# Kernel optimization log

Hardware: AMD Instinct MI355X
Metric: run time of the kernel (lower is better)

## Reference

```python
import jax, jax.numpy as jnp
import numpy as np

CODEBOOK_SIZE = 8192
HIDDEN_SIZE = 256
N_ANCHORS = 5


def setup_inputs() -> dict:
    key = jax.random.key(0)
    k1, k2 = jax.random.split(key)
    z = jax.random.normal(k1, (8, 4096, HIDDEN_SIZE), dtype=jnp.float32)
    emb = 0.02 * jax.random.normal(k2, (CODEBOOK_SIZE, HIDDEN_SIZE), dtype=jnp.float32)
    # enforce_anchor_values(): first 5 rows are one-hot anchors (eye padded with zeros)
    anchors = jnp.zeros((N_ANCHORS, HIDDEN_SIZE), dtype=jnp.float32)
    anchors = anchors.at[:, :N_ANCHORS].set(jnp.eye(N_ANCHORS, dtype=jnp.float32))
    emb = emb.at[:N_ANCHORS, :].set(anchors)
    return {"z": z, "emb": emb}


def reference(z, emb):
    b, t, h = z.shape
    flat = z.reshape(b * t, h)
    # squared L2 distance: ||z||^2 - 2 z.e + ||e||^2  -> [b*t, K]
    dist = (
        jnp.sum(flat * flat, axis=1, keepdims=True)
        - 2.0 * (flat @ emb.T)
        + jnp.sum(emb * emb, axis=1)[None, :]
    )
    idx = jnp.argmin(dist, axis=1)  # [b*t]
    z_q = emb[idx].reshape(b, t, h)
    # straight-through estimator
    z_st = z + jax.lax.stop_gradient(z_q - z)
    codebook_loss = jnp.mean((z_q - jax.lax.stop_gradient(z)) ** 2)
    commit_loss = jnp.mean((z - jax.lax.stop_gradient(z_q)) ** 2)
    return z_st, idx.reshape(b, t), codebook_loss, commit_loss
```

## Files before the change

kernel.cpp:

```cpp
#include <hip/hip_runtime.h>

#define HIDDEN 256
#define K_CODES 8192
#define N_TOK 32768
#define ZST_ELEMS 8388608
#define N_ANCHORS 5
#define NCH 64
#define MARGIN 8.0e-3f
#define WLS_CAP 131072
#define WLC_CAP 131072
#define EPI_BLOCKS 8192

using short8 = __attribute__((ext_vector_type(8))) short;
using f32x4  = __attribute__((ext_vector_type(4))) float;

__device__ __forceinline__ unsigned short f2bf(float f) {
    unsigned int u = __float_as_uint(f);
    return (unsigned short)((u + 0x7fffu + ((u >> 16) & 1u)) >> 16);
}

__device__ __forceinline__ void gl2lds16(const void* g, void* l) {
    __builtin_amdgcn_global_load_lds(
        (const __attribute__((address_space(1))) unsigned int*)g,
        (__attribute__((address_space(3))) unsigned int*)l, 16, 0, 0);
}

__device__ __forceinline__ unsigned long long score_key(float s, int code) {
    unsigned int u = __float_as_uint(s);
    u = (u & 0x80000000u) ? ~u : (u | 0x80000000u);
    return (((unsigned long long)u) << 32) | (unsigned int)code;
}

__global__ void prep_kernel(const float* __restrict__ emb, const float* __restrict__ z,
                            float* __restrict__ ne, float* __restrict__ zn,
                            unsigned short* __restrict__ Bh, unsigned short* __restrict__ Ah) {
#pragma clang fp contract(off)
    int gt  = blockIdx.x * 256 + threadIdx.x;
    int row = gt >> 4;
    int sub = gt & 15;
    const float* src; unsigned short* dst; float* nrm;
    if (row < K_CODES) {
        src = emb + (size_t)row * HIDDEN;
        dst = Bh  + (size_t)row * HIDDEN;
        nrm = ne + row;
    } else {
        int r2 = row - K_CODES;
        src = z  + (size_t)r2 * HIDDEN;
        dst = Ah + (size_t)r2 * HIDDEN;
        nrm = zn + r2;
    }
    const float* p = src + (sub >> 3) * 128 + (sub & 7);
    float v = p[0];
    float r = v * v;
    #pragma unroll
    for (int i = 1; i < 16; ++i) { float w = p[8 * i]; r += w * w; }
    r += __shfl_xor(r, 1, 64);
    r += __shfl_xor(r, 2, 64);
    r += __shfl_xor(r, 4, 64);
    r += __shfl_xor(r, 8, 64);
    if (sub == 0) *nrm = r;

    const float4* s4 = (const float4*)src + sub * 4;
    #pragma unroll
    for (int j = 0; j < 2; ++j) {
        float4 a = s4[2 * j];
        float4 b = s4[2 * j + 1];
        short8 h;
        h[0] = (short)f2bf(a.x); h[1] = (short)f2bf(a.y);
        h[2] = (short)f2bf(a.z); h[3] = (short)f2bf(a.w);
        h[4] = (short)f2bf(b.x); h[5] = (short)f2bf(b.y);
        h[6] = (short)f2bf(b.z); h[7] = (short)f2bf(b.w);
        *(short8*)(dst + sub * 16 + j * 8) = h;
    }
}

__global__ __launch_bounds__(512, 4) void mfma_score_kernel(
    const unsigned short* __restrict__ Ah,
    const unsigned short* __restrict__ Bh,
    const float* __restrict__ ne,
    float* __restrict__ p1, float* __restrict__ p2, unsigned short* __restrict__ piu) {

    __shared__ unsigned short Ahs[2][256 * 32];
    __shared__ unsigned short Bhs[2][128 * 32];

    const int tid  = threadIdx.x;
    const int wm   = tid >> 6;
    const int lane = tid & 63;
    const int L    = lane & 15;
    const int q    = lane >> 4;

    const int lin  = blockIdx.x;
    const int xcd  = lin & 7;
    const int s    = lin >> 3;
    const int nb   = s >> 4;
    const int m0   = (xcd * 16 + (s & 15)) * 256;
    const int n0   = nb * 128;

    f32x4 acc[2][8] = {};

    auto STAGE = [&](int kt, int buf) {
        const int k0 = kt * 32;
        #pragma unroll
        for (int r = 0; r < 2; ++r) {
            int u   = tid + 512 * r;
            int row = u >> 2;
            int p   = u & 3;
            int ch  = p ^ ((row >> 1) & 3);
            gl2lds16(Ah + (size_t)(m0 + row) * HIDDEN + k0 + ch * 8,
                     &Ahs[buf][u * 8]);
        }
        {
            int u   = tid;
            int row = u >> 2;
            int p   = u & 3;
            int ch  = p ^ ((row >> 1) & 3);
            gl2lds16(Bh + (size_t)(n0 + row) * HIDDEN + k0 + ch * 8,
                     &Bhs[buf][u * 8]);
        }
    };

    STAGE(0, 0);
    __syncthreads();

    #pragma unroll
    for (int kt = 0; kt < 8; ++kt) {
        const int cur = kt & 1;
        if (kt < 7) STAGE(kt + 1, cur ^ 1);

        const short8* A8h = (const short8*)Ahs[cur];
        const short8* B8h = (const short8*)Bhs[cur];

        short8 ah[2];
        #pragma unroll
        for (int tm = 0; tm < 2; ++tm) {
            int m  = wm * 32 + tm * 16 + L;
            ah[tm] = A8h[m * 4 + (q ^ ((m >> 1) & 3))];
        }
        #pragma unroll
        for (int tn = 0; tn < 8; ++tn) {
            int n  = tn * 16 + L;
            short8 bh = B8h[n * 4 + (q ^ ((n >> 1) & 3))];
            #pragma unroll
            for (int tm = 0; tm < 2; ++tm) {
                acc[tm][tn] = __builtin_amdgcn_mfma_f32_16x16x32_bf16(
                    ah[tm], bh, acc[tm][tn], 0, 0, 0);
            }
        }
        if (kt < 7) __syncthreads();
    }

    float nev[8];
    #pragma unroll
    for (int tn = 0; tn < 8; ++tn) nev[tn] = ne[n0 + tn * 16 + L];
    if (nb == 0 && L < N_ANCHORS) nev[0] = 3.4e38f;

    #pragma unroll
    for (int tm = 0; tm < 2; ++tm) {
        #pragma unroll
        for (int reg = 0; reg < 4; ++reg) {
            float m1 = 3.4e38f, m2 = 3.4e38f;
            int bi = 0;
            #pragma unroll
            for (int tn = 0; tn < 8; ++tn) {
                float s2 = nev[tn] - 2.0f * acc[tm][tn][reg];
                int lo = tn * 16 + L;
                if (s2 < m1)      { m2 = m1; m1 = s2; bi = lo; }
                else if (s2 < m2) { m2 = s2; }
            }
            #pragma unroll
            for (int off = 1; off < 16; off <<= 1) {
                float o1 = __shfl_xor(m1, off, 64);
                float o2 = __shfl_xor(m2, off, 64);
                int   oi = __shfl_xor(bi, off, 64);
                if (o1 < m1 || (o1 == m1 && oi < bi)) {
                    m2 = fminf(m1, o2); m1 = o1; bi = oi;
                } else {
                    m2 = fminf(m2, o1);
                }
            }
            if (L == 0) {
                size_t mrow = (size_t)m0 + wm * 32 + tm * 16 + q * 4 + reg;
                p1[(size_t)nb * N_TOK + mrow]  = m1;
                p2[(size_t)nb * N_TOK + mrow]  = m2;
                piu[(size_t)nb * N_TOK + mrow] = (unsigned short)bi;
            }
        }
    }
}

__global__ void combine_kernel(const float* __restrict__ p1, const float* __restrict__ p2,
                               const unsigned short* __restrict__ piu,
                               const float* __restrict__ z, const float* __restrict__ zn,
                               const float* __restrict__ ne,
                               float* __restrict__ idxf, int* __restrict__ flags,
                               unsigned long long* __restrict__ slots,
                               int* __restrict__ wls, int* __restrict__ wlc,
                               unsigned int* __restrict__ wcnt) {
#pragma clang fp contract(off)
    int t = blockIdx.x * 256 + threadIdx.x;
    float m1 = 3.4e38f, m2 = 3.4e38f;
    int bi = 0;
    for (int nb = 0; nb < NCH; ++nb) {
        float o1 = p1[(size_t)nb * N_TOK + t];
        float o2 = p2[(size_t)nb * N_TOK + t];
        if (o1 < m1) {
            m2 = fminf(m1, o2); m1 = o1;
            bi = nb * 128 + (int)piu[(size_t)nb * N_TOK + t];
        } else {
            m2 = fminf(m2, o1);
        }
    }
    float zt = zn[t];
    const float* zp = z + (size_t)t * HIDDEN;
    float sa = 3.4e38f; int ai = 0;
    #pragma unroll
    for (int a = 0; a < N_ANCHORS; ++a) {
        float s = (zt - 2.0f * zp[a]) + ne[a];
        if (s < sa) { sa = s; ai = a; }
    }
    slots[t] = score_key(sa, ai);
    float g = sa - zt;
    bool anchorWin = (g + MARGIN < m1);
    bool amb = !anchorWin && ((m2 - m1 < MARGIN) || (g <= m1 + MARGIN));
    idxf[t]  = anchorWin ? (float)ai : (float)bi;
    flags[t] = amb ? 1 : 0;
    if (amb) {
        float thr = m1 + MARGIN;
        for (int nb = 0; nb < NCH; ++nb) {
            float o1 = p1[(size_t)nb * N_TOK + t];
            if (o1 <= thr) {
                if (p2[(size_t)nb * N_TOK + t] <= thr) {
                    unsigned int pos = atomicAdd(&wcnt[1], 2u);
                    if (pos + 1 < WLC_CAP) {
                        wlc[pos]     = (t << 7) | (nb * 2);
                        wlc[pos + 1] = (t << 7) | (nb * 2 + 1);
                    }
                } else {
                    unsigned int pos = atomicAdd(&wcnt[0], 1u);
                    if (pos < WLS_CAP)
                        wls[pos] = (t << 13) | (nb * 128 + (int)piu[(size_t)nb * N_TOK + t]);
                }
            }
        }
    }
}

__global__ __launch_bounds__(256) void rescue_single(
    const float* __restrict__ z, const float* __restrict__ emb,
    const float* __restrict__ ne, const float* __restrict__ zn,
    const int* __restrict__ wls, const unsigned int* __restrict__ wcnt,
    unsigned long long* __restrict__ slots) {
#pragma clang fp contract(off)
    int ns = (int)wcnt[0];
    if (ns > WLS_CAP) ns = WLS_CAP;
    for (int i = blockIdx.x * 256 + threadIdx.x; i < ns; i += gridDim.x * 256) {
        int it = wls[i];
        int t  = it >> 13;
        int c  = it & (K_CODES - 1);
        const float4* zp = (const float4*)(z + (size_t)t * HIDDEN);
        const float4* ep = (const float4*)(emb + (size_t)c * HIDDEN);
        float acc = 0.0f;
        #pragma unroll 8
        for (int k4 = 0; k4 < 64; ++k4) {
            float4 zv = zp[k4];
            float4 ev = ep[k4];
            acc = __builtin_fmaf(ev.x, zv.x, acc);
            acc = __builtin_fmaf(ev.y, zv.y, acc);
            acc = __builtin_fmaf(ev.z, zv.z, acc);
            acc = __builtin_fmaf(ev.w, zv.w, acc);
        }
        float s = (zn[t] - 2.0f * acc) + ne[c];
        atomicMin(&slots[t], score_key(s, c));
    }
}

__global__ __launch_bounds__(64) void rescue_scan(
    const float* __restrict__ z, const float* __restrict__ emb,
    const float* __restrict__ ne, const float* __restrict__ zn,
    const int* __restrict__ wlc, const unsigned int* __restrict__ wcnt,
    unsigned long long* __restrict__ slots) {
#pragma clang fp contract(off)
    __shared__ float zs[HIDDEN];

    int nit = (int)wcnt[1];
    if (nit > WLC_CAP) nit = WLC_CAP;

    for (int item = blockIdx.x; item < nit; item += gridDim.x) {
        int w   = wlc[item];
        int t   = w >> 7;
        int nb2 = w & 127;
        __syncthreads();
        ((float4*)zs)[threadIdx.x] = ((const float4*)(z + (size_t)t * HIDDEN))[threadIdx.x];
        __syncthreads();

        int c = nb2 * 64 + threadIdx.x;
        const float4* e4 = (const float4*)(emb + (size_t)c * HIDDEN);
        float acc = 0.0f;
        #pragma unroll 8
        for (int k4 = 0; k4 < 64; ++k4) {
            float4 ev = e4[k4];
            acc = __builtin_fmaf(ev.x, zs[k4 * 4 + 0], acc);
            acc = __builtin_fmaf(ev.y, zs[k4 * 4 + 1], acc);
            acc = __builtin_fmaf(ev.z, zs[k4 * 4 + 2], acc);
            acc = __builtin_fmaf(ev.w, zs[k4 * 4 + 3], acc);
        }
        float t1 = zn[t] - 2.0f * acc;
        float s  = t1 + ne[c];

        unsigned long long key = score_key(s, c);
        #pragma unroll
        for (int off = 1; off < 64; off <<= 1) {
            unsigned long long o = __shfl_xor(key, off, 64);
            if (o < key) key = o;
        }
        if (threadIdx.x == 0) atomicMin(&slots[t], key);
    }
}

__global__ void epilogue_kernel(const float* __restrict__ z, const float* __restrict__ emb,
                                const int* __restrict__ flags,
                                const unsigned long long* __restrict__ slots,
                                float* __restrict__ idxf, float* __restrict__ zst,
                                float* __restrict__ loss_part) {
    int t4    = blockIdx.x * 256 + threadIdx.x;
    int token = t4 >> 6;
    int k4    = t4 & 63;

    int idx;
    if (flags[token]) idx = (int)(unsigned int)(slots[token] & 0xFFFFFFFFULL);
    else              idx = (int)idxf[token];
    if (k4 == 0) idxf[token] = (float)idx;

    float4 zv = ((const float4*)z)[t4];
    float4 ev = ((const float4*)emb)[(size_t)idx * 64 + k4];

    float dx = ev.x - zv.x, dy = ev.y - zv.y, dz = ev.z - zv.z, dw = ev.w - zv.w;
    float4 o = { zv.x + dx, zv.y + dy, zv.z + dz, zv.w + dw };
    ((float4*)zst)[t4] = o;

    float p = dx * dx + dy * dy + dz * dz + dw * dw;
    #pragma unroll
    for (int off = 32; off; off >>= 1) p += __shfl_down(p, off, 64);

    __shared__ float wsum[4];
    int lane = threadIdx.x & 63, w = threadIdx.x >> 6;
    if (lane == 0) wsum[w] = p;
    __syncthreads();
    if (threadIdx.x == 0)
        loss_part[blockIdx.x] = wsum[0] + wsum[1] + wsum[2] + wsum[3];
}

__global__ __launch_bounds__(256) void finalize_kernel(
    const float* __restrict__ loss_part, float* __restrict__ out_losses) {
    float s = 0.0f;
    for (int i = threadIdx.x; i < EPI_BLOCKS; i += 256) s += loss_part[i];
    #pragma unroll
    for (int off = 32; off; off >>= 1) s += __shfl_down(s, off, 64);
    __shared__ float ws[4];
    int lane = threadIdx.x & 63, w = threadIdx.x >> 6;
    if (lane == 0) ws[w] = s;
    __syncthreads();
    if (threadIdx.x == 0) {
        float m = (ws[0] + ws[1] + ws[2] + ws[3]) * (1.0f / (float)ZST_ELEMS);
        out_losses[0] = m;
        out_losses[1] = m;
    }
}

extern "C" void kernel_launch(void* const* d_in, const int* in_sizes, int n_in,
                              void* d_out, int out_size, void* d_ws, size_t ws_size,
                              hipStream_t stream) {
    const float* z   = (const float*)d_in[0];
    const float* emb = (const float*)d_in[1];

    float* out    = (float*)d_out;
    float* zst    = out;
    float* idxf   = out + ZST_ELEMS;
    float* losses = out + ZST_ELEMS + N_TOK;

    char* w = (char*)d_ws;
    unsigned short* Ah = (unsigned short*)w;    w += (size_t)N_TOK  * HIDDEN * 2;
    unsigned short* Bh = (unsigned short*)w;    w += (size_t)K_CODES * HIDDEN * 2;
    float* p1 = (float*)w;                      w += (size_t)NCH * N_TOK * 4;
    float* p2 = (float*)w;                      w += (size_t)NCH * N_TOK * 4;
    unsigned short* piu = (unsigned short*)w;   w += (size_t)NCH * N_TOK * 2;
    float* ne = (float*)w;                      w += K_CODES * 4;
    float* zn = (float*)w;                      w += N_TOK * 4;
    int*   flags = (int*)w;                     w += N_TOK * 4;
    unsigned long long* slots = (unsigned long long*)w;  w += N_TOK * 8;
    int*   wls = (int*)w;                       w += (size_t)WLS_CAP * 4;
    int*   wlc = (int*)w;                       w += (size_t)WLC_CAP * 4;
    float* loss_part = (float*)w;               w += (size_t)EPI_BLOCKS * 4;
    unsigned int* wcnt = (unsigned int*)w;

    hipMemsetAsync(wcnt, 0, 8, stream);
    prep_kernel<<<(K_CODES + N_TOK) * 16 / 256, 256, 0, stream>>>(emb, z, ne, zn, Bh, Ah);
    mfma_score_kernel<<<N_TOK / 256 * NCH, 512, 0, stream>>>(Ah, Bh, ne, p1, p2, piu);
    combine_kernel<<<N_TOK / 256, 256, 0, stream>>>(p1, p2, piu, z, zn, ne,
                                                    idxf, flags, slots, wls, wlc, wcnt);
    rescue_single<<<512, 256, 0, stream>>>(z, emb, ne, zn, wls, wcnt, slots);
    rescue_scan<<<2048, 64, 0, stream>>>(z, emb, ne, zn, wlc, wcnt, slots);
    epilogue_kernel<<<EPI_BLOCKS, 256, 0, stream>>>(z, emb, flags, slots,
                                                    idxf, zst, loss_part);
    finalize_kernel<<<1, 256, 0, stream>>>(loss_part, losses);
}
```

Baseline: 438.2 us.

## Prefetch two K-tiles ahead in MFMA score kernel and fuse rescue kernels

The MFMA score kernel now issues loads for the next two K-stages up front and uses explicit vmcnt waits with raw barriers, so global-to-LDS copies overlap more with the MFMA work. The two rescue kernels are merged into one launch. The scan part now assigns one wavefront per work item and reads z directly from global memory instead of staging it in shared memory behind block barriers. This removes one kernel launch and the per-item syncs, but it relies on hand-tuned vmcnt counts, which could be wrong or racy if the number of loads per stage changes.

```diff
diff --git a/kernel.cpp b/kernel.cpp
--- a/kernel.cpp
+++ b/kernel.cpp
@@ -120,12 +120,14 @@
     };
 
     STAGE(0, 0);
-    __syncthreads();
+    STAGE(1, 1);
+    asm volatile("s_waitcnt vmcnt(3)" ::: "memory");
+    __builtin_amdgcn_s_barrier();
+    asm volatile("" ::: "memory");
 
     #pragma unroll
     for (int kt = 0; kt < 8; ++kt) {
         const int cur = kt & 1;
-        if (kt < 7) STAGE(kt + 1, cur ^ 1);
 
         const short8* A8h = (const short8*)Ahs[cur];
         const short8* B8h = (const short8*)Bhs[cur];
@@ -146,7 +148,19 @@
                     ah[tm], bh, acc[tm][tn], 0, 0, 0);
             }
         }
-        if (kt < 7) __syncthreads();
+
+        if (kt < 7) {
+            __builtin_amdgcn_s_barrier();
+            asm volatile("" ::: "memory");
+            if (kt + 2 < 8) {
+                STAGE(kt + 2, cur);
+                asm volatile("s_waitcnt vmcnt(3)" ::: "memory");
+            } else {
+                asm volatile("s_waitcnt vmcnt(0)" ::: "memory");
+            }
+            __builtin_amdgcn_s_barrier();
+            asm volatile("" ::: "memory");
+        }
     }
 
     float nev[8];
@@ -245,10 +259,11 @@
     }
 }
 
-__global__ __launch_bounds__(256) void rescue_single(
+__global__ __launch_bounds__(256) void rescue_fused(
     const float* __restrict__ z, const float* __restrict__ emb,
     const float* __restrict__ ne, const float* __restrict__ zn,
-    const int* __restrict__ wls, const unsigned int* __restrict__ wcnt,
+    const int* __restrict__ wls, const int* __restrict__ wlc,
+    const unsigned int* __restrict__ wcnt,
     unsigned long long* __restrict__ slots) {
 #pragma clang fp contract(off)
     int ns = (int)wcnt[0];
@@ -272,37 +287,29 @@
         float s = (zn[t] - 2.0f * acc) + ne[c];
         atomicMin(&slots[t], score_key(s, c));
     }
-}
-
-__global__ __launch_bounds__(64) void rescue_scan(
-    const float* __restrict__ z, const float* __restrict__ emb,
-    const float* __restrict__ ne, const float* __restrict__ zn,
-    const int* __restrict__ wlc, const unsigned int* __restrict__ wcnt,
-    unsigned long long* __restrict__ slots) {
-#pragma clang fp contract(off)
-    __shared__ float zs[HIDDEN];
 
     int nit = (int)wcnt[1];
     if (nit > WLC_CAP) nit = WLC_CAP;
-
-    for (int item = blockIdx.x; item < nit; item += gridDim.x) {
+    const int lane = threadIdx.x & 63;
+    const int wid  = (blockIdx.x * 256 + threadIdx.x) >> 6;
+    const int nw   = gridDim.x * 4;
+
+    for (int item = wid; item < nit; item += nw) {
         int w   = wlc[item];
         int t   = w >> 7;
         int nb2 = w & 127;
-        __syncthreads();
-        ((float4*)zs)[threadIdx.x] = ((const float4*)(z + (size_t)t * HIDDEN))[threadIdx.x];
-        __syncthreads();
-
-        int c = nb2 * 64 + threadIdx.x;
-        const float4* e4 = (const float4*)(emb + (size_t)c * HIDDEN);
+        int c   = nb2 * 64 + lane;
+        const float4* e4  = (const float4*)(emb + (size_t)c * HIDDEN);
+        const float4* zp4 = (const float4*)(z + (size_t)t * HIDDEN);
         float acc = 0.0f;
         #pragma unroll 8
         for (int k4 = 0; k4 < 64; ++k4) {
+            float4 zv = zp4[k4];
             float4 ev = e4[k4];
-            acc = __builtin_fmaf(ev.x, zs[k4 * 4 + 0], acc);
-            acc = __builtin_fmaf(ev.y, zs[k4 * 4 + 1], acc);
-            acc = __builtin_fmaf(ev.z, zs[k4 * 4 + 2], acc);
-            acc = __builtin_fmaf(ev.w, zs[k4 * 4 + 3], acc);
+            acc = __builtin_fmaf(ev.x, zv.x, acc);
+            acc = __builtin_fmaf(ev.y, zv.y, acc);
+            acc = __builtin_fmaf(ev.z, zv.z, acc);
+            acc = __builtin_fmaf(ev.w, zv.w, acc);
         }
         float t1 = zn[t] - 2.0f * acc;
         float s  = t1 + ne[c];
@@ -313,7 +320,7 @@
             unsigned long long o = __shfl_xor(key, off, 64);
             if (o < key) key = o;
         }
-        if (threadIdx.x == 0) atomicMin(&slots[t], key);
+        if (lane == 0) atomicMin(&slots[t], key);
     }
 }
 
@@ -398,8 +405,7 @@
     mfma_score_kernel<<<N_TOK / 256 * NCH, 512, 0, stream>>>(Ah, Bh, ne, p1, p2, piu);
     combine_kernel<<<N_TOK / 256, 256, 0, stream>>>(p1, p2, piu, z, zn, ne,
                                                     idxf, flags, slots, wls, wlc, wcnt);
-    rescue_single<<<512, 256, 0, stream>>>(z, emb, ne, zn, wls, wcnt, slots);
-    rescue_scan<<<2048, 64, 0, stream>>>(z, emb, ne, zn, wlc, wcnt, slots);
+    rescue_fused<<<1024, 256, 0, stream>>>(z, emb, ne, zn, wls, wlc, wcnt, slots);
     epilogue_kernel<<<EPI_BLOCKS, 256, 0, stream>>>(z, emb, flags, slots,
                                                     idxf, zst, loss_part);
     finalize_kernel<<<1, 256, 0, stream>>>(loss_part, losses);
```

Measured after the change: 436.4 us. No clear change (-0.4%).
